# Kernel optimization log

Measured on AMD Instinct MI355X. Metric: run time of the kernel, lower is better.

## Reference

```python
import jax, jax.numpy as jnp
import numpy as np

HIDDEN = 1024
ATTN = 1024
B, L = 16, 1024


def setup_inputs() -> dict:
    key = jax.random.key(0)
    ks = jax.random.split(key, 9)
    s = 1.0 / np.sqrt(HIDDEN)
    return {
        "meme_features": jax.random.normal(ks[0], (B, L, HIDDEN), jnp.float32),
        "text_features": jax.random.normal(ks[1], (B, L, HIDDEN), jnp.float32),
        "emoji_features": jax.random.normal(ks[2], (B, L, HIDDEN), jnp.float32),
        # nn.Linear params: weight [out, in], bias [out]
        "Wq": jax.random.uniform(ks[3], (ATTN, HIDDEN), jnp.float32, -s, s),
        "bq": jax.random.uniform(ks[4], (ATTN,), jnp.float32, -s, s),
        "Wk": jax.random.uniform(ks[5], (ATTN, HIDDEN), jnp.float32, -s, s),
        "bk": jax.random.uniform(ks[6], (ATTN,), jnp.float32, -s, s),
        "Wv": jax.random.uniform(ks[7], (ATTN, HIDDEN), jnp.float32, -s, s),
        "bv": jax.random.uniform(ks[8], (ATTN,), jnp.float32, -s, s),
    }


def reference(meme_features, text_features, emoji_features, Wq, bq, Wk, bk, Wv, bv):
    # Linear projections (x @ W^T + b)
    q = jnp.einsum("blh,ah->bla", meme_features, Wq) + bq   # [B, Lq, A]
    k = jnp.einsum("blh,ah->bla", text_features, Wk) + bk   # [B, Lk, A]
    v = jnp.einsum("blh,ah->bla", emoji_features, Wv) + bv  # [B, Lk, A]
    # NOTE: original module has NO 1/sqrt(d) scaling and NO mask.
    scores = jnp.einsum("bqa,bka->bqk", q, k)               # [B, Lq, Lk]
    weights = jax.nn.softmax(scores, axis=-1)
    return jnp.einsum("bqk,bka->bqa", weights, v)           # [B, Lq, A]
```

## Files before the change

### kernel.cpp

```cpp
#include <hip/hip_runtime.h>

typedef _Float16 half8_t __attribute__((ext_vector_type(8)));
typedef _Float16 half4_t __attribute__((ext_vector_type(4)));
typedef float floatx4 __attribute__((ext_vector_type(4)));

__device__ inline void gload16(const void* g, void* l) {
  __builtin_amdgcn_global_load_lds(
      (const __attribute__((address_space(1))) unsigned int*)g,
      (__attribute__((address_space(3))) unsigned int*)l, 16, 0, 0);
}

constexpr int NT = 16;

template <int MH>
__device__ inline void lda_frags(const char* sA, int wr, int quad, int mrow,
                                 half8_t af[4][2]) {
#pragma unroll
  for (int mf = 0; mf < 4; ++mf)
#pragma unroll
    for (int kk = 0; kk < 2; ++kk)
      af[mf][kk] = *(const half8_t*)(
          sA + (size_t)(((kk * 4 + quad) * 256 + MH * 128 + wr * 64 +
                         mf * 16 + mrow) << 4));
}

template <int NH>
__device__ inline void ldb_frags(const char* sB, int wc, int quad, int mrow,
                                 half8_t bf[2][2]) {
#pragma unroll
  for (int nf = 0; nf < 2; ++nf)
#pragma unroll
    for (int kk = 0; kk < 2; ++kk)
      bf[nf][kk] = *(const half8_t*)(
          sB + (size_t)(((kk * 4 + quad) * 256 + NH * 128 + wc * 32 +
                         nf * 16 + mrow) << 4));
}

template <int MH, int NH>
__device__ inline void mfma_quad(const half8_t af[4][2], const half8_t bf[2][2],
                                 floatx4 acc[8][4]) {
  __builtin_amdgcn_s_setprio(1);
#pragma unroll
  for (int mf = 0; mf < 4; ++mf)
#pragma unroll
    for (int nf = 0; nf < 2; ++nf)
#pragma unroll
      for (int kk = 0; kk < 2; ++kk)
        acc[MH * 4 + mf][NH * 2 + nf] = __builtin_amdgcn_mfma_f32_16x16x32_f16(
            af[mf][kk], bf[nf][kk], acc[MH * 4 + mf][NH * 2 + nf], 0, 0, 0);
  __builtin_amdgcn_s_setprio(0);
}

__device__ inline void stage_half(const _Float16* __restrict__ X, int ldx,
                                  int u, char* opbase, int h, int wid,
                                  int lane) {
#pragma unroll
  for (int i = 0; i < 2; ++i) {
    gload16(X + (long)(h * 128 + i * 64 + lane) * ldx + u * 64 + wid * 8,
            opbase + (size_t)((wid * 256 + h * 128 + i * 64) << 4));
  }
}

template <typename OT, int BIAS, int GX, int GY>
__global__ __launch_bounds__(512, 2) void gemm256(
    const _Float16* __restrict__ A, long As, int lda,
    const _Float16* __restrict__ B, long Bs, int ldb,
    OT* __restrict__ C, long Cs, int ldc,
    const float* __restrict__ bias, int biasStride) {
  __shared__ char smem[131072];

  const int id = blockIdx.x;
  const int chunk = gridDim.x >> 3;
  const int nid = (id & 7) * chunk + (id >> 3);
  const int bx = nid % GX;
  const int by = (nid / GX) % GY;
  const int bz = nid / (GX * GY);

  const int tid = threadIdx.x;
  const int lane = tid & 63;
  const int wid = tid >> 6;
  const int wr = wid >> 2;
  const int wc = wid & 3;
  const int quad = lane >> 4;
  const int mrow = lane & 15;
  const long m0 = (long)by * 256;
  const long n0 = (long)bx * 256;
  const _Float16* Ab = A + (long)bz * As + m0 * (long)lda;
  const _Float16* Bb = B + (long)bz * Bs + n0 * (long)ldb;
  C += (long)bz * Cs;

  floatx4 acc[8][4] = {};
  half8_t af[4][2], bf[2][2];

  {
    char* sA0 = smem;
    char* sB0 = smem + 65536;
    char* sA1 = smem + 32768;
    char* sB1 = smem + 65536 + 32768;
    stage_half(Ab, lda, 0, sA0, 0, wid, lane);
    stage_half(Bb, ldb, 0, sB0, 1, wid, lane);
    stage_half(Ab, lda, 0, sA0, 1, wid, lane);
    stage_half(Bb, ldb, 0, sB0, 0, wid, lane);
    stage_half(Ab, lda, 1, sA1, 0, wid, lane);
    stage_half(Bb, ldb, 1, sB1, 1, wid, lane);
    stage_half(Ab, lda, 1, sA1, 1, wid, lane);
    asm volatile("s_waitcnt vmcnt(6)" ::: "memory");
    __builtin_amdgcn_s_barrier();
  }

  for (int t = 0; t < NT; ++t) {
    const int p = t & 1, q = p ^ 1;
    char* sAp = smem + p * 32768;
    char* sBp = smem + 65536 + p * 32768;
    char* sBq = smem + 65536 + q * 32768;
    const int u1 = (t + 1 < NT) ? t + 1 : NT - 1;
    const int u2 = (t + 2 < NT) ? t + 2 : NT - 1;

    lda_frags<0>(sAp, wr, quad, mrow, af);
    ldb_frags<0>(sBp, wc, quad, mrow, bf);
    stage_half(Bb, ldb, u1, sBq, 0, wid, lane);
    __builtin_amdgcn_s_barrier();
    asm volatile("s_waitcnt lgkmcnt(0)" ::: "memory");
    mfma_quad<0, 0>(af, bf, acc);
    __builtin_amdgcn_s_barrier();

    ldb_frags<1>(sBp, wc, quad, mrow, bf);
    stage_half(Ab, lda, u2, sAp, 0, wid, lane);
    __builtin_amdgcn_s_barrier();
    asm volatile("s_waitcnt lgkmcnt(0)" ::: "memory");
    mfma_quad<0, 1>(af, bf, acc);
    __builtin_amdgcn_s_barrier();

    lda_frags<1>(sAp, wr, quad, mrow, af);
    stage_half(Bb, ldb, u2, sBp, 1, wid, lane);
    __builtin_amdgcn_s_barrier();
    asm volatile("s_waitcnt lgkmcnt(0)" ::: "memory");
    mfma_quad<1, 1>(af, bf, acc);
    __builtin_amdgcn_s_barrier();

    ldb_frags<0>(sBp, wc, quad, mrow, bf);
    stage_half(Ab, lda, u2, sAp, 1, wid, lane);
    asm volatile("s_waitcnt vmcnt(6)" ::: "memory");
    __builtin_amdgcn_s_barrier();
    asm volatile("s_waitcnt lgkmcnt(0)" ::: "memory");
    mfma_quad<1, 0>(af, bf, acc);
    __builtin_amdgcn_s_barrier();
  }

  asm volatile("s_waitcnt vmcnt(0)" ::: "memory");

#pragma unroll
  for (int mh = 0; mh < 2; ++mh)
#pragma unroll
    for (int mf = 0; mf < 4; ++mf) {
      const int rbase = mh * 128 + wr * 64 + mf * 16 + quad * 4;
#pragma unroll
      for (int nh = 0; nh < 2; ++nh)
#pragma unroll
        for (int nf = 0; nf < 2; ++nf) {
          const int cc = (int)n0 + nh * 128 + wc * 32 + nf * 16 + mrow;
#pragma unroll
          for (int r = 0; r < 4; ++r) {
            const long row = m0 + rbase + r;
            float v = acc[mh * 4 + mf][nh * 2 + nf][r];
            if constexpr (BIAS == 1) v += bias[bz * biasStride + cc];
            if constexpr (BIAS == 2) v += bias[(int)row];
            C[row * (long)ldc + cc] = (OT)v;
          }
        }
    }
}


__global__ __launch_bounds__(256) void convert_x(const float* __restrict__ x0,
                                                 const float* __restrict__ x1,
                                                 const float* __restrict__ x2,
                                                 _Float16* __restrict__ out) {
  int i = blockIdx.x * 256 + threadIdx.x;
  int t = i >> 22;
  int j = i & 4194303;
  const float* src = (t == 0) ? x0 : (t == 1) ? x1 : x2;
  floatx4 v = ((const floatx4*)src)[j];
  half4_t h = {(_Float16)v[0], (_Float16)v[1], (_Float16)v[2], (_Float16)v[3]};
  ((half4_t*)out)[i] = h;
}

__global__ __launch_bounds__(256) void convert_w(const float* __restrict__ Wq,
                                                 const float* __restrict__ Wk,
                                                 const float* __restrict__ Wv,
                                                 _Float16* __restrict__ out) {
  int i = blockIdx.x * 256 + threadIdx.x;
  int t = i >> 18;
  int j = i & 262143;
  const float* src = (t == 0) ? Wq : (t == 1) ? Wk : Wv;
  floatx4 v = ((const floatx4*)src)[j];
  half4_t h = {(_Float16)v[0], (_Float16)v[1], (_Float16)v[2], (_Float16)v[3]};
  ((half4_t*)out)[i] = h;
}

__global__ __launch_bounds__(256) void pack_bias(const float* __restrict__ bq,
                                                 const float* __restrict__ bk,
                                                 const float* __restrict__ bv,
                                                 float* __restrict__ out) {
  int b = blockIdx.x;
  const float* src = (b == 0) ? bq : (b == 1) ? bk : bv;
  ((floatx4*)out)[b * 256 + threadIdx.x] =
      ((const floatx4*)src)[threadIdx.x];
}

__global__ __launch_bounds__(256) void softmax_rows_h(_Float16* __restrict__ S) {
  long row = blockIdx.x;
  _Float16* Sr = S + row * 1024;
  int tid = threadIdx.x, lane = tid & 63, wid = tid >> 6;
  half4_t x = ((const half4_t*)Sr)[tid];
  float x0 = x[0], x1 = x[1], x2 = x[2], x3 = x[3];
  float mx = fmaxf(fmaxf(x0, x1), fmaxf(x2, x3));
#pragma unroll
  for (int off = 32; off > 0; off >>= 1) mx = fmaxf(mx, __shfl_xor(mx, off));
  __shared__ float redm[4];
  if (lane == 0) redm[wid] = mx;
  __syncthreads();
  mx = fmaxf(fmaxf(redm[0], redm[1]), fmaxf(redm[2], redm[3]));
  float e0 = __expf(x0 - mx), e1 = __expf(x1 - mx);
  float e2 = __expf(x2 - mx), e3 = __expf(x3 - mx);
  float s = e0 + e1 + e2 + e3;
#pragma unroll
  for (int off = 32; off > 0; off >>= 1) s += __shfl_xor(s, off);
  __shared__ float reds[4];
  if (lane == 0) reds[wid] = s;
  __syncthreads();
  s = reds[0] + reds[1] + reds[2] + reds[3];
  float inv = 1.0f / s;
  half4_t h = {(_Float16)(e0 * inv), (_Float16)(e1 * inv),
               (_Float16)(e2 * inv), (_Float16)(e3 * inv)};
  ((half4_t*)Sr)[tid] = h;
}

extern "C" void kernel_launch(void* const* d_in, const int* in_sizes, int n_in,
                              void* d_out, int out_size, void* d_ws,
                              size_t ws_size, hipStream_t stream) {
  (void)in_sizes; (void)n_in; (void)out_size; (void)ws_size;
  const float* meme  = (const float*)d_in[0];
  const float* text  = (const float*)d_in[1];
  const float* emoji = (const float*)d_in[2];
  const float* Wq = (const float*)d_in[3];
  const float* bq = (const float*)d_in[4];
  const float* Wk = (const float*)d_in[5];
  const float* bk = (const float*)d_in[6];
  const float* Wv = (const float*)d_in[7];
  const float* bv = (const float*)d_in[8];

  const long MB = 1024 * 1024;
  char* ws = (char*)d_ws;
  _Float16* hWq = (_Float16*)ws;
  float* pbias  = (float*)(ws + 6 * MB);
  _Float16* mh  = (_Float16*)(ws + 7 * MB);
  _Float16* th  = (_Float16*)(ws + 39 * MB);
  _Float16* eh  = (_Float16*)(ws + 71 * MB);
  _Float16* Qh  = (_Float16*)(ws + 103 * MB);
  _Float16* Kh  = (_Float16*)(ws + 135 * MB);
  _Float16* S   = mh;
  _Float16* Vt  = th;
  _Float16* hWv = hWq + 2 * MB;

  dim3 blk(256), blk5(512);
  convert_w<<<3072, blk, 0, stream>>>(Wq, Wk, Wv, hWq);
  pack_bias<<<3, blk, 0, stream>>>(bq, bk, bv, pbias);
  convert_x<<<49152, blk, 0, stream>>>(meme, text, emoji, mh);

  gemm256<_Float16, 1, 4, 64><<<dim3(512), blk5, 0, stream>>>(
      mh, 16777216, 1024, hWq, 1048576, 1024, Qh, 16777216, 1024, pbias, 1024);
  gemm256<_Float16, 2, 64, 4><<<dim3(256), blk5, 0, stream>>>(
      hWv, 0, 1024, eh, 0, 1024, Vt, 0, 16384, pbias + 2048, 0);
  gemm256<_Float16, 0, 4, 4><<<dim3(256), blk5, 0, stream>>>(
      Qh, 1048576, 1024, Kh, 1048576, 1024, S, 1048576, 1024, nullptr, 0);
  softmax_rows_h<<<16384, blk, 0, stream>>>(S);
  gemm256<float, 0, 4, 4><<<dim3(256), blk5, 0, stream>>>(
      S, 1048576, 1024, Vt, 1024, 16384, (float*)d_out, 1048576, 1024,
      nullptr, 0);
}
```

Before: 472.6 us.

## Software-pipeline GEMM main loop with per-k-half fragments and fewer barriers

```diff
diff --git a/kernel.cpp b/kernel.cpp
--- a/kernel.cpp
+++ b/kernel.cpp
@@ -12,42 +12,34 @@
 
 constexpr int NT = 16;
 
-template <int MH>
-__device__ inline void lda_frags(const char* sA, int wr, int quad, int mrow,
-                                 half8_t af[4][2]) {
+__device__ inline void lda1(const char* sA, int kk, int qm, int wr, int quad,
+                            int mrow, half8_t af[4]) {
 #pragma unroll
   for (int mf = 0; mf < 4; ++mf)
-#pragma unroll
-    for (int kk = 0; kk < 2; ++kk)
-      af[mf][kk] = *(const half8_t*)(
-          sA + (size_t)(((kk * 4 + quad) * 256 + MH * 128 + wr * 64 +
-                         mf * 16 + mrow) << 4));
-}
-
-template <int NH>
-__device__ inline void ldb_frags(const char* sB, int wc, int quad, int mrow,
-                                 half8_t bf[2][2]) {
+    af[mf] = *(const half8_t*)(
+        sA + (size_t)(((kk * 4 + quad) * 256 + qm * 128 + wr * 64 + mf * 16 +
+                       mrow) << 4));
+}
+
+__device__ inline void ldb1(const char* sB, int kk, int qn, int wc, int quad,
+                            int mrow, half8_t bf[2]) {
 #pragma unroll
   for (int nf = 0; nf < 2; ++nf)
-#pragma unroll
-    for (int kk = 0; kk < 2; ++kk)
-      bf[nf][kk] = *(const half8_t*)(
-          sB + (size_t)(((kk * 4 + quad) * 256 + NH * 128 + wc * 32 +
-                         nf * 16 + mrow) << 4));
-}
-
-template <int MH, int NH>
-__device__ inline void mfma_quad(const half8_t af[4][2], const half8_t bf[2][2],
-                                 floatx4 acc[8][4]) {
+    bf[nf] = *(const half8_t*)(
+        sB + (size_t)(((kk * 4 + quad) * 256 + qn * 128 + wc * 32 + nf * 16 +
+                       mrow) << 4));
+}
+
+template <int QM, int QN>
+__device__ inline void mfma8(const half8_t af[4], const half8_t bf[2],
+                             floatx4 acc[8][4]) {
   __builtin_amdgcn_s_setprio(1);
 #pragma unroll
   for (int mf = 0; mf < 4; ++mf)
 #pragma unroll
     for (int nf = 0; nf < 2; ++nf)
-#pragma unroll
-      for (int kk = 0; kk < 2; ++kk)
-        acc[MH * 4 + mf][NH * 2 + nf] = __builtin_amdgcn_mfma_f32_16x16x32_f16(
-            af[mf][kk], bf[nf][kk], acc[MH * 4 + mf][NH * 2 + nf], 0, 0, 0);
+      acc[QM * 4 + mf][QN * 2 + nf] = __builtin_amdgcn_mfma_f32_16x16x32_f16(
+          af[mf], bf[nf], acc[QM * 4 + mf][QN * 2 + nf], 0, 0, 0);
   __builtin_amdgcn_s_setprio(0);
 }
 
@@ -90,7 +82,7 @@
   C += (long)bz * Cs;
 
   floatx4 acc[8][4] = {};
-  half8_t af[4][2], bf[2][2];
+  half8_t af_a[4], af_b[4], bfA[2], bfB[2];
 
   {
     char* sA0 = smem;
@@ -98,53 +90,55 @@
     char* sA1 = smem + 32768;
     char* sB1 = smem + 65536 + 32768;
     stage_half(Ab, lda, 0, sA0, 0, wid, lane);
-    stage_half(Bb, ldb, 0, sB0, 1, wid, lane);
     stage_half(Ab, lda, 0, sA0, 1, wid, lane);
     stage_half(Bb, ldb, 0, sB0, 0, wid, lane);
+    stage_half(Bb, ldb, 0, sB0, 1, wid, lane);
     stage_half(Ab, lda, 1, sA1, 0, wid, lane);
+    stage_half(Ab, lda, 1, sA1, 1, wid, lane);
+    stage_half(Bb, ldb, 1, sB1, 0, wid, lane);
     stage_half(Bb, ldb, 1, sB1, 1, wid, lane);
-    stage_half(Ab, lda, 1, sA1, 1, wid, lane);
-    asm volatile("s_waitcnt vmcnt(6)" ::: "memory");
-    __builtin_amdgcn_s_barrier();
+    asm volatile("s_waitcnt vmcnt(8)" ::: "memory");
+    __builtin_amdgcn_s_barrier();
+    lda1(sA0, 0, 0, wr, quad, mrow, af_a);
+    ldb1(sB0, 0, 0, wc, quad, mrow, bfA);
   }
 
   for (int t = 0; t < NT; ++t) {
     const int p = t & 1, q = p ^ 1;
-    char* sAp = smem + p * 32768;
-    char* sBp = smem + 65536 + p * 32768;
-    char* sBq = smem + 65536 + q * 32768;
-    const int u1 = (t + 1 < NT) ? t + 1 : NT - 1;
-    const int u2 = (t + 2 < NT) ? t + 2 : NT - 1;
-
-    lda_frags<0>(sAp, wr, quad, mrow, af);
-    ldb_frags<0>(sBp, wc, quad, mrow, bf);
-    stage_half(Bb, ldb, u1, sBq, 0, wid, lane);
-    __builtin_amdgcn_s_barrier();
+    char* sAc = smem + p * 32768;
+    char* sBc = smem + 65536 + p * 32768;
+    char* sAn = smem + q * 32768;
+    char* sBn = smem + 65536 + q * 32768;
+    const int tu = (t + 2 < NT) ? t + 2 : NT - 1;
+
+    ldb1(sBc, 0, 1, wc, quad, mrow, bfB);
+    mfma8<0, 0>(af_a, bfA, acc);
+    lda1(sAc, 0, 1, wr, quad, mrow, af_b);
+    mfma8<0, 1>(af_a, bfB, acc);
+    mfma8<1, 1>(af_b, bfB, acc);
+    lda1(sAc, 1, 1, wr, quad, mrow, af_a);
+    ldb1(sBc, 1, 0, wc, quad, mrow, bfB);
+    mfma8<1, 0>(af_b, bfA, acc);
     asm volatile("s_waitcnt lgkmcnt(0)" ::: "memory");
-    mfma_quad<0, 0>(af, bf, acc);
-    __builtin_amdgcn_s_barrier();
-
-    ldb_frags<1>(sBp, wc, quad, mrow, bf);
-    stage_half(Ab, lda, u2, sAp, 0, wid, lane);
-    __builtin_amdgcn_s_barrier();
+    __builtin_amdgcn_s_barrier();
+    stage_half(Ab, lda, tu, sAc, 1, wid, lane);
+    stage_half(Bb, ldb, tu, sBc, 0, wid, lane);
+    ldb1(sBc, 1, 1, wc, quad, mrow, bfA);
+    mfma8<1, 0>(af_a, bfB, acc);
     asm volatile("s_waitcnt lgkmcnt(0)" ::: "memory");
-    mfma_quad<0, 1>(af, bf, acc);
-    __builtin_amdgcn_s_barrier();
-
-    lda_frags<1>(sAp, wr, quad, mrow, af);
-    stage_half(Bb, ldb, u2, sBp, 1, wid, lane);
-    __builtin_amdgcn_s_barrier();
+    __builtin_amdgcn_s_barrier();
+    stage_half(Bb, ldb, tu, sBc, 1, wid, lane);
+    lda1(sAc, 1, 0, wr, quad, mrow, af_b);
+    mfma8<1, 1>(af_a, bfA, acc);
     asm volatile("s_waitcnt lgkmcnt(0)" ::: "memory");
-    mfma_quad<1, 1>(af, bf, acc);
-    __builtin_amdgcn_s_barrier();
-
-    ldb_frags<0>(sBp, wc, quad, mrow, bf);
-    stage_half(Ab, lda, u2, sAp, 1, wid, lane);
-    asm volatile("s_waitcnt vmcnt(6)" ::: "memory");
-    __builtin_amdgcn_s_barrier();
-    asm volatile("s_waitcnt lgkmcnt(0)" ::: "memory");
-    mfma_quad<1, 0>(af, bf, acc);
-    __builtin_amdgcn_s_barrier();
+    __builtin_amdgcn_s_barrier();
+    stage_half(Ab, lda, tu, sAc, 0, wid, lane);
+    mfma8<0, 1>(af_b, bfA, acc);
+    asm volatile("s_waitcnt vmcnt(8)" ::: "memory");
+    __builtin_amdgcn_s_barrier();
+    lda1(sAn, 0, 0, wr, quad, mrow, af_a);
+    ldb1(sBn, 0, 0, wc, quad, mrow, bfA);
+    mfma8<0, 0>(af_b, bfB, acc);
   }
 
   asm volatile("s_waitcnt vmcnt(0)" ::: "memory");
```

Result: slower. 482.3 us (+2.0%).

## Fuse fp32-to-fp16 conversion of Q/K inputs into GEMM and switch to 32x32 MFMA

Applied to the files above, without the earlier changes.

```diff
diff --git a/kernel.cpp b/kernel.cpp
--- a/kernel.cpp
+++ b/kernel.cpp
@@ -3,6 +3,7 @@
 typedef _Float16 half8_t __attribute__((ext_vector_type(8)));
 typedef _Float16 half4_t __attribute__((ext_vector_type(4)));
 typedef float floatx4 __attribute__((ext_vector_type(4)));
+typedef float f32x16 __attribute__((ext_vector_type(16)));
 
 __device__ inline void gload16(const void* g, void* l) {
   __builtin_amdgcn_global_load_lds(
@@ -13,41 +14,36 @@
 constexpr int NT = 16;
 
 template <int MH>
-__device__ inline void lda_frags(const char* sA, int wr, int quad, int mrow,
-                                 half8_t af[4][2]) {
-#pragma unroll
-  for (int mf = 0; mf < 4; ++mf)
-#pragma unroll
-    for (int kk = 0; kk < 2; ++kk)
-      af[mf][kk] = *(const half8_t*)(
-          sA + (size_t)(((kk * 4 + quad) * 256 + MH * 128 + wr * 64 +
-                         mf * 16 + mrow) << 4));
+__device__ inline void lda_frags(const char* sA, int wr, int lo, int hi,
+                                 half8_t af[2][4]) {
+#pragma unroll
+  for (int mp = 0; mp < 2; ++mp)
+#pragma unroll
+    for (int ks = 0; ks < 4; ++ks)
+      af[mp][ks] = *(const half8_t*)(
+          sA + (size_t)(((ks * 2 + hi) * 256 + MH * 128 + wr * 64 + mp * 32 +
+                         lo) << 4));
 }
 
 template <int NH>
-__device__ inline void ldb_frags(const char* sB, int wc, int quad, int mrow,
-                                 half8_t bf[2][2]) {
-#pragma unroll
-  for (int nf = 0; nf < 2; ++nf)
-#pragma unroll
-    for (int kk = 0; kk < 2; ++kk)
-      bf[nf][kk] = *(const half8_t*)(
-          sB + (size_t)(((kk * 4 + quad) * 256 + NH * 128 + wc * 32 +
-                         nf * 16 + mrow) << 4));
-}
-
-template <int MH, int NH>
-__device__ inline void mfma_quad(const half8_t af[4][2], const half8_t bf[2][2],
-                                 floatx4 acc[8][4]) {
+__device__ inline void ldb_frags(const char* sB, int wc, int lo, int hi,
+                                 half8_t bf[4]) {
+#pragma unroll
+  for (int ks = 0; ks < 4; ++ks)
+    bf[ks] = *(const half8_t*)(
+        sB + (size_t)(((ks * 2 + hi) * 256 + NH * 128 + wc * 32 + lo) << 4));
+}
+
+template <int MQ, int NI>
+__device__ inline void mfma_quad(const half8_t af[2][4], const half8_t bf[4],
+                                 f32x16 acc[4][2]) {
   __builtin_amdgcn_s_setprio(1);
 #pragma unroll
-  for (int mf = 0; mf < 4; ++mf)
-#pragma unroll
-    for (int nf = 0; nf < 2; ++nf)
-#pragma unroll
-      for (int kk = 0; kk < 2; ++kk)
-        acc[MH * 4 + mf][NH * 2 + nf] = __builtin_amdgcn_mfma_f32_16x16x32_f16(
-            af[mf][kk], bf[nf][kk], acc[MH * 4 + mf][NH * 2 + nf], 0, 0, 0);
+  for (int mp = 0; mp < 2; ++mp)
+#pragma unroll
+    for (int ks = 0; ks < 4; ++ks)
+      acc[MQ + mp][NI] = __builtin_amdgcn_mfma_f32_32x32x16_f16(
+          af[mp][ks], bf[ks], acc[MQ + mp][NI], 0, 0, 0);
   __builtin_amdgcn_s_setprio(0);
 }
 
@@ -61,12 +57,38 @@
   }
 }
 
-template <typename OT, int BIAS, int GX, int GY>
+__device__ inline void a32_issue(const float* __restrict__ X, int ldx, int u,
+                                 int wid, int lane, floatx4 va[4][2]) {
+#pragma unroll
+  for (int hj = 0; hj < 4; ++hj) {
+    const float* src =
+        X + (long)((hj >> 1) * 128 + (hj & 1) * 64 + lane) * ldx + u * 64 +
+        wid * 8;
+    va[hj][0] = *(const floatx4*)(src);
+    va[hj][1] = *(const floatx4*)(src + 4);
+  }
+}
+
+__device__ inline void a32_write(char* opbase, int wid, int lane,
+                                 const floatx4 va[4][2]) {
+#pragma unroll
+  for (int hj = 0; hj < 4; ++hj) {
+    half8_t h = {(_Float16)va[hj][0][0], (_Float16)va[hj][0][1],
+                 (_Float16)va[hj][0][2], (_Float16)va[hj][0][3],
+                 (_Float16)va[hj][1][0], (_Float16)va[hj][1][1],
+                 (_Float16)va[hj][1][2], (_Float16)va[hj][1][3]};
+    *(half8_t*)(opbase +
+                (size_t)((wid * 256 + (hj >> 1) * 128 + (hj & 1) * 64 + lane)
+                         << 4)) = h;
+  }
+}
+
+template <typename OT, int BIAS, int GX, int GY, int ACVT>
 __global__ __launch_bounds__(512, 2) void gemm256(
-    const _Float16* __restrict__ A, long As, int lda,
-    const _Float16* __restrict__ B, long Bs, int ldb,
-    OT* __restrict__ C, long Cs, int ldc,
-    const float* __restrict__ bias, int biasStride) {
+    const _Float16* __restrict__ A, const float* __restrict__ A32, long As,
+    int lda, const _Float16* __restrict__ B, long Bs, int ldb,
+    OT* __restrict__ C, long Cs, int ldc, const float* __restrict__ bias,
+    int biasStride) {
   __shared__ char smem[131072];
 
   const int id = blockIdx.x;
@@ -81,22 +103,38 @@
   const int wid = tid >> 6;
   const int wr = wid >> 2;
   const int wc = wid & 3;
-  const int quad = lane >> 4;
-  const int mrow = lane & 15;
+  const int lo = lane & 31;
+  const int hi = lane >> 5;
   const long m0 = (long)by * 256;
   const long n0 = (long)bx * 256;
-  const _Float16* Ab = A + (long)bz * As + m0 * (long)lda;
+  const _Float16* Ab = A;
+  const float* A32b = A32;
+  if constexpr (ACVT) A32b += (long)bz * As + m0 * (long)lda;
+  else Ab += (long)bz * As + m0 * (long)lda;
   const _Float16* Bb = B + (long)bz * Bs + n0 * (long)ldb;
   C += (long)bz * Cs;
 
-  floatx4 acc[8][4] = {};
-  half8_t af[4][2], bf[2][2];
-
-  {
-    char* sA0 = smem;
-    char* sB0 = smem + 65536;
-    char* sA1 = smem + 32768;
-    char* sB1 = smem + 65536 + 32768;
+  f32x16 acc[4][2] = {};
+  half8_t af[2][4], bf0[4], bf1[4];
+  floatx4 va[4][2];
+
+  char* sA0 = smem;
+  char* sA1 = smem + 32768;
+  char* sB0 = smem + 65536;
+  char* sB1 = smem + 65536 + 32768;
+
+  if constexpr (ACVT) {
+    a32_issue(A32b, lda, 0, wid, lane, va);
+    stage_half(Bb, ldb, 0, sB0, 0, wid, lane);
+    stage_half(Bb, ldb, 0, sB0, 1, wid, lane);
+    stage_half(Bb, ldb, 1, sB1, 1, wid, lane);
+    asm volatile("s_waitcnt vmcnt(6)" ::: "memory");
+    a32_write(sA0, wid, lane, va);
+    a32_issue(A32b, lda, 1, wid, lane, va);
+    asm volatile("s_waitcnt vmcnt(0)" ::: "memory");
+    a32_write(sA1, wid, lane, va);
+    __syncthreads();
+  } else {
     stage_half(Ab, lda, 0, sA0, 0, wid, lane);
     stage_half(Bb, ldb, 0, sB0, 1, wid, lane);
     stage_half(Ab, lda, 0, sA0, 1, wid, lane);
@@ -110,77 +148,75 @@
 
   for (int t = 0; t < NT; ++t) {
     const int p = t & 1, q = p ^ 1;
-    char* sAp = smem + p * 32768;
-    char* sBp = smem + 65536 + p * 32768;
+    char* sAc = smem + p * 32768;
+    char* sBc = smem + 65536 + p * 32768;
     char* sBq = smem + 65536 + q * 32768;
     const int u1 = (t + 1 < NT) ? t + 1 : NT - 1;
     const int u2 = (t + 2 < NT) ? t + 2 : NT - 1;
 
-    lda_frags<0>(sAp, wr, quad, mrow, af);
-    ldb_frags<0>(sBp, wc, quad, mrow, bf);
+    lda_frags<0>(sAc, wr, lo, hi, af);
+    ldb_frags<0>(sBc, wc, lo, hi, bf0);
     stage_half(Bb, ldb, u1, sBq, 0, wid, lane);
     __builtin_amdgcn_s_barrier();
     asm volatile("s_waitcnt lgkmcnt(0)" ::: "memory");
-    mfma_quad<0, 0>(af, bf, acc);
-    __builtin_amdgcn_s_barrier();
-
-    ldb_frags<1>(sBp, wc, quad, mrow, bf);
-    stage_half(Ab, lda, u2, sAp, 0, wid, lane);
+    mfma_quad<0, 0>(af, bf0, acc);
+    __builtin_amdgcn_s_barrier();
+
+    ldb_frags<1>(sBc, wc, lo, hi, bf1);
+    if constexpr (ACVT)
+      a32_issue(A32b, lda, u2, wid, lane, va);
+    else
+      stage_half(Ab, lda, u2, sAc, 0, wid, lane);
     __builtin_amdgcn_s_barrier();
     asm volatile("s_waitcnt lgkmcnt(0)" ::: "memory");
-    mfma_quad<0, 1>(af, bf, acc);
-    __builtin_amdgcn_s_barrier();
-
-    lda_frags<1>(sAp, wr, quad, mrow, af);
-    stage_half(Bb, ldb, u2, sBp, 1, wid, lane);
+    mfma_quad<0, 1>(af, bf1, acc);
+    __builtin_amdgcn_s_barrier();
+
+    lda_frags<1>(sAc, wr, lo, hi, af);
+    stage_half(Bb, ldb, u2, sBc, 1, wid, lane);
     __builtin_amdgcn_s_barrier();
     asm volatile("s_waitcnt lgkmcnt(0)" ::: "memory");
-    mfma_quad<1, 1>(af, bf, acc);
-    __builtin_amdgcn_s_barrier();
-
-    ldb_frags<0>(sBp, wc, quad, mrow, bf);
-    stage_half(Ab, lda, u2, sAp, 1, wid, lane);
-    asm volatile("s_waitcnt vmcnt(6)" ::: "memory");
+    mfma_quad<2, 1>(af, bf1, acc);
+    __builtin_amdgcn_s_barrier();
+
+    if constexpr (ACVT) {
+      asm volatile("s_waitcnt vmcnt(2)" ::: "memory");
+      a32_write(sAc, wid, lane, va);
+    } else {
+      stage_half(Ab, lda, u2, sAc, 1, wid, lane);
+      asm volatile("s_waitcnt vmcnt(6)" ::: "memory");
+    }
     __builtin_amdgcn_s_barrier();
     asm volatile("s_waitcnt lgkmcnt(0)" ::: "memory");
-    mfma_quad<1, 0>(af, bf, acc);
+    mfma_quad<2, 0>(af, bf0, acc);
     __builtin_amdgcn_s_barrier();
   }
 
   asm volatile("s_waitcnt vmcnt(0)" ::: "memory");
 
 #pragma unroll
-  for (int mh = 0; mh < 2; ++mh)
-#pragma unroll
-    for (int mf = 0; mf < 4; ++mf) {
-      const int rbase = mh * 128 + wr * 64 + mf * 16 + quad * 4;
-#pragma unroll
-      for (int nh = 0; nh < 2; ++nh)
-#pragma unroll
-        for (int nf = 0; nf < 2; ++nf) {
-          const int cc = (int)n0 + nh * 128 + wc * 32 + nf * 16 + mrow;
-#pragma unroll
-          for (int r = 0; r < 4; ++r) {
-            const long row = m0 + rbase + r;
-            float v = acc[mh * 4 + mf][nh * 2 + nf][r];
-            if constexpr (BIAS == 1) v += bias[bz * biasStride + cc];
-            if constexpr (BIAS == 2) v += bias[(int)row];
-            C[row * (long)ldc + cc] = (OT)v;
-          }
-        }
+  for (int mi = 0; mi < 4; ++mi) {
+    const int r0 = (mi >> 1) * 128 + wr * 64 + (mi & 1) * 32 + 4 * hi;
+#pragma unroll
+    for (int ni = 0; ni < 2; ++ni) {
+      const int cc = (int)n0 + ni * 128 + wc * 32 + lo;
+#pragma unroll
+      for (int e = 0; e < 16; ++e) {
+        const long row = m0 + r0 + (e & 3) + 8 * (e >> 2);
+        float v = acc[mi][ni][e];
+        if constexpr (BIAS == 1) v += bias[bz * biasStride + cc];
+        if constexpr (BIAS == 2) v += bias[(int)row];
+        C[row * (long)ldc + cc] = (OT)v;
+      }
     }
-}
-
-
-__global__ __launch_bounds__(256) void convert_x(const float* __restrict__ x0,
-                                                 const float* __restrict__ x1,
-                                                 const float* __restrict__ x2,
+  }
+}
+
+
+__global__ __launch_bounds__(256) void convert_e(const float* __restrict__ x,
                                                  _Float16* __restrict__ out) {
   int i = blockIdx.x * 256 + threadIdx.x;
-  int t = i >> 22;
-  int j = i & 4194303;
-  const float* src = (t == 0) ? x0 : (t == 1) ? x1 : x2;
-  floatx4 v = ((const floatx4*)src)[j];
+  floatx4 v = ((const floatx4*)x)[i];
   half4_t h = {(_Float16)v[0], (_Float16)v[1], (_Float16)v[2], (_Float16)v[3]};
   ((half4_t*)out)[i] = h;
 }
@@ -254,28 +290,30 @@
   char* ws = (char*)d_ws;
   _Float16* hWq = (_Float16*)ws;
   float* pbias  = (float*)(ws + 6 * MB);
-  _Float16* mh  = (_Float16*)(ws + 7 * MB);
-  _Float16* th  = (_Float16*)(ws + 39 * MB);
+  _Float16* S   = (_Float16*)(ws + 7 * MB);
+  _Float16* Vt  = (_Float16*)(ws + 39 * MB);
   _Float16* eh  = (_Float16*)(ws + 71 * MB);
   _Float16* Qh  = (_Float16*)(ws + 103 * MB);
   _Float16* Kh  = (_Float16*)(ws + 135 * MB);
-  _Float16* S   = mh;
-  _Float16* Vt  = th;
+  _Float16* hWk = hWq + 1 * MB;
   _Float16* hWv = hWq + 2 * MB;
 
   dim3 blk(256), blk5(512);
   convert_w<<<3072, blk, 0, stream>>>(Wq, Wk, Wv, hWq);
   pack_bias<<<3, blk, 0, stream>>>(bq, bk, bv, pbias);
-  convert_x<<<49152, blk, 0, stream>>>(meme, text, emoji, mh);
-
-  gemm256<_Float16, 1, 4, 64><<<dim3(512), blk5, 0, stream>>>(
-      mh, 16777216, 1024, hWq, 1048576, 1024, Qh, 16777216, 1024, pbias, 1024);
-  gemm256<_Float16, 2, 64, 4><<<dim3(256), blk5, 0, stream>>>(
-      hWv, 0, 1024, eh, 0, 1024, Vt, 0, 16384, pbias + 2048, 0);
-  gemm256<_Float16, 0, 4, 4><<<dim3(256), blk5, 0, stream>>>(
-      Qh, 1048576, 1024, Kh, 1048576, 1024, S, 1048576, 1024, nullptr, 0);
+  convert_e<<<16384, blk, 0, stream>>>(emoji, eh);
+
+  gemm256<_Float16, 1, 4, 64, 1><<<dim3(256), blk5, 0, stream>>>(
+      nullptr, meme, 0, 1024, hWq, 0, 1024, Qh, 0, 1024, pbias, 0);
+  gemm256<_Float16, 1, 4, 64, 1><<<dim3(256), blk5, 0, stream>>>(
+      nullptr, text, 0, 1024, hWk, 0, 1024, Kh, 0, 1024, pbias + 1024, 0);
+  gemm256<_Float16, 2, 64, 4, 0><<<dim3(256), blk5, 0, stream>>>(
+      hWv, nullptr, 0, 1024, eh, 0, 1024, Vt, 0, 16384, pbias + 2048, 0);
+  gemm256<_Float16, 0, 4, 4, 0><<<dim3(256), blk5, 0, stream>>>(
+      Qh, nullptr, 1048576, 1024, Kh, 1048576, 1024, S, 1048576, 1024,
+      nullptr, 0);
   softmax_rows_h<<<16384, blk, 0, stream>>>(S);
-  gemm256<float, 0, 4, 4><<<dim3(256), blk5, 0, stream>>>(
-      S, 1048576, 1024, Vt, 1024, 16384, (float*)d_out, 1048576, 1024,
-      nullptr, 0);
-}
+  gemm256<float, 0, 4, 4, 0><<<dim3(256), blk5, 0, stream>>>(
+      S, nullptr, 1048576, 1024, Vt, 1024, 16384, (float*)d_out, 1048576,
+      1024, nullptr, 0);
+}
```

Result: slower. 509.0 us (+7.7%).

## Switch GEMM to 32x32x16 MFMA with XOR-swizzled LDS layout

Applied to the files above, without the earlier changes.

```diff
diff --git a/kernel.cpp b/kernel.cpp
--- a/kernel.cpp
+++ b/kernel.cpp
@@ -3,6 +3,7 @@
 typedef _Float16 half8_t __attribute__((ext_vector_type(8)));
 typedef _Float16 half4_t __attribute__((ext_vector_type(4)));
 typedef float floatx4 __attribute__((ext_vector_type(4)));
+typedef float f32x16 __attribute__((ext_vector_type(16)));
 
 __device__ inline void gload16(const void* g, void* l) {
   __builtin_amdgcn_global_load_lds(
@@ -12,52 +13,44 @@
 
 constexpr int NT = 16;
 
-template <int MH>
-__device__ inline void lda_frags(const char* sA, int wr, int quad, int mrow,
-                                 half8_t af[4][2]) {
-#pragma unroll
-  for (int mf = 0; mf < 4; ++mf)
-#pragma unroll
-    for (int kk = 0; kk < 2; ++kk)
-      af[mf][kk] = *(const half8_t*)(
-          sA + (size_t)(((kk * 4 + quad) * 256 + MH * 128 + wr * 64 +
-                         mf * 16 + mrow) << 4));
-}
-
-template <int NH>
-__device__ inline void ldb_frags(const char* sB, int wc, int quad, int mrow,
-                                 half8_t bf[2][2]) {
-#pragma unroll
-  for (int nf = 0; nf < 2; ++nf)
-#pragma unroll
-    for (int kk = 0; kk < 2; ++kk)
-      bf[nf][kk] = *(const half8_t*)(
-          sB + (size_t)(((kk * 4 + quad) * 256 + NH * 128 + wc * 32 +
-                         nf * 16 + mrow) << 4));
-}
-
-template <int MH, int NH>
-__device__ inline void mfma_quad(const half8_t af[4][2], const half8_t bf[2][2],
-                                 floatx4 acc[8][4]) {
+__device__ inline void lda_frags2(const char* sA, int rb, const int* xk,
+                                  half8_t af[2][4]) {
+#pragma unroll
+  for (int mp = 0; mp < 2; ++mp)
+#pragma unroll
+    for (int ks = 0; ks < 4; ++ks)
+      af[mp][ks] = *(const half8_t*)(
+          sA + (size_t)((rb + mp * 32) * 128 + xk[ks] * 16));
+}
+
+__device__ inline void ldb_frags2(const char* sB, int cb, const int* xk,
+                                  half8_t bf[4]) {
+#pragma unroll
+  for (int ks = 0; ks < 4; ++ks)
+    bf[ks] = *(const half8_t*)(sB + (size_t)(cb * 128 + xk[ks] * 16));
+}
+
+template <int MQ, int NI>
+__device__ inline void mfma_quad(const half8_t af[2][4], const half8_t bf[4],
+                                 f32x16 acc[4][2]) {
   __builtin_amdgcn_s_setprio(1);
 #pragma unroll
-  for (int mf = 0; mf < 4; ++mf)
-#pragma unroll
-    for (int nf = 0; nf < 2; ++nf)
-#pragma unroll
-      for (int kk = 0; kk < 2; ++kk)
-        acc[MH * 4 + mf][NH * 2 + nf] = __builtin_amdgcn_mfma_f32_16x16x32_f16(
-            af[mf][kk], bf[nf][kk], acc[MH * 4 + mf][NH * 2 + nf], 0, 0, 0);
+  for (int mp = 0; mp < 2; ++mp)
+#pragma unroll
+    for (int ks = 0; ks < 4; ++ks)
+      acc[MQ + mp][NI] = __builtin_amdgcn_mfma_f32_32x32x16_f16(
+          af[mp][ks], bf[ks], acc[MQ + mp][NI], 0, 0, 0);
   __builtin_amdgcn_s_setprio(0);
 }
 
-__device__ inline void stage_half(const _Float16* __restrict__ X, int ldx,
-                                  int u, char* opbase, int h, int wid,
-                                  int lane) {
+__device__ inline void stage_half(const _Float16* __restrict__ X, long laneoff,
+                                  int ldx, int u, char* opbase, int h,
+                                  int wid) {
 #pragma unroll
   for (int i = 0; i < 2; ++i) {
-    gload16(X + (long)(h * 128 + i * 64 + lane) * ldx + u * 64 + wid * 8,
-            opbase + (size_t)((wid * 256 + h * 128 + i * 64) << 4));
+    const int c0 = h * 1024 + wid * 128 + i * 64;
+    gload16(X + (long)(c0 >> 3) * ldx + u * 64 + laneoff,
+            opbase + (size_t)c0 * 16);
   }
 }
 
@@ -65,8 +58,8 @@
 __global__ __launch_bounds__(512, 2) void gemm256(
     const _Float16* __restrict__ A, long As, int lda,
     const _Float16* __restrict__ B, long Bs, int ldb,
-    OT* __restrict__ C, long Cs, int ldc,
-    const float* __restrict__ bias, int biasStride) {
+    OT* __restrict__ C, long Cs, int ldc, const float* __restrict__ bias,
+    int biasStride) {
   __shared__ char smem[131072];
 
   const int id = blockIdx.x;
@@ -81,94 +74,96 @@
   const int wid = tid >> 6;
   const int wr = wid >> 2;
   const int wc = wid & 3;
-  const int quad = lane >> 4;
-  const int mrow = lane & 15;
+  const int lo = lane & 31;
+  const int hi = lane >> 5;
+  const int l7 = lane & 7;
+  const int l8 = lane >> 3;
+  const long laneA = (long)l8 * lda + ((l7 ^ l8) << 3);
+  const long laneB = (long)l8 * ldb + ((l7 ^ l8) << 3);
+  int xk[4];
+#pragma unroll
+  for (int ks = 0; ks < 4; ++ks) xk[ks] = (ks * 2 + hi) ^ l7;
+
   const long m0 = (long)by * 256;
   const long n0 = (long)bx * 256;
   const _Float16* Ab = A + (long)bz * As + m0 * (long)lda;
   const _Float16* Bb = B + (long)bz * Bs + n0 * (long)ldb;
   C += (long)bz * Cs;
 
-  floatx4 acc[8][4] = {};
-  half8_t af[4][2], bf[2][2];
-
-  {
-    char* sA0 = smem;
-    char* sB0 = smem + 65536;
-    char* sA1 = smem + 32768;
-    char* sB1 = smem + 65536 + 32768;
-    stage_half(Ab, lda, 0, sA0, 0, wid, lane);
-    stage_half(Bb, ldb, 0, sB0, 1, wid, lane);
-    stage_half(Ab, lda, 0, sA0, 1, wid, lane);
-    stage_half(Bb, ldb, 0, sB0, 0, wid, lane);
-    stage_half(Ab, lda, 1, sA1, 0, wid, lane);
-    stage_half(Bb, ldb, 1, sB1, 1, wid, lane);
-    stage_half(Ab, lda, 1, sA1, 1, wid, lane);
-    asm volatile("s_waitcnt vmcnt(6)" ::: "memory");
-    __builtin_amdgcn_s_barrier();
-  }
+  f32x16 acc[4][2] = {};
+  half8_t af[2][4], bf0[4], bf1[4];
+
+  char* sA0 = smem;
+  char* sA1 = smem + 32768;
+  char* sB0 = smem + 65536;
+  char* sB1 = smem + 65536 + 32768;
+
+  stage_half(Ab, laneA, lda, 0, sA0, 0, wid);
+  stage_half(Bb, laneB, ldb, 0, sB0, 1, wid);
+  stage_half(Ab, laneA, lda, 0, sA0, 1, wid);
+  stage_half(Bb, laneB, ldb, 0, sB0, 0, wid);
+  stage_half(Ab, laneA, lda, 1, sA1, 0, wid);
+  stage_half(Bb, laneB, ldb, 1, sB1, 1, wid);
+  stage_half(Ab, laneA, lda, 1, sA1, 1, wid);
+  asm volatile("s_waitcnt vmcnt(6)" ::: "memory");
+  __builtin_amdgcn_s_barrier();
 
   for (int t = 0; t < NT; ++t) {
     const int p = t & 1, q = p ^ 1;
-    char* sAp = smem + p * 32768;
-    char* sBp = smem + 65536 + p * 32768;
+    char* sAc = smem + p * 32768;
+    char* sBc = smem + 65536 + p * 32768;
     char* sBq = smem + 65536 + q * 32768;
     const int u1 = (t + 1 < NT) ? t + 1 : NT - 1;
     const int u2 = (t + 2 < NT) ? t + 2 : NT - 1;
 
-    lda_frags<0>(sAp, wr, quad, mrow, af);
-    ldb_frags<0>(sBp, wc, quad, mrow, bf);
-    stage_half(Bb, ldb, u1, sBq, 0, wid, lane);
-    __builtin_amdgcn_s_barrier();
-    asm volatile("s_waitcnt lgkmcnt(0)" ::: "memory");
-    mfma_quad<0, 0>(af, bf, acc);
-    __builtin_amdgcn_s_barrier();
-
-    ldb_frags<1>(sBp, wc, quad, mrow, bf);
-    stage_half(Ab, lda, u2, sAp, 0, wid, lane);
-    __builtin_amdgcn_s_barrier();
-    asm volatile("s_waitcnt lgkmcnt(0)" ::: "memory");
-    mfma_quad<0, 1>(af, bf, acc);
-    __builtin_amdgcn_s_barrier();
-
-    lda_frags<1>(sAp, wr, quad, mrow, af);
-    stage_half(Bb, ldb, u2, sBp, 1, wid, lane);
-    __builtin_amdgcn_s_barrier();
-    asm volatile("s_waitcnt lgkmcnt(0)" ::: "memory");
-    mfma_quad<1, 1>(af, bf, acc);
-    __builtin_amdgcn_s_barrier();
-
-    ldb_frags<0>(sBp, wc, quad, mrow, bf);
-    stage_half(Ab, lda, u2, sAp, 1, wid, lane);
+    lda_frags2(sAc, wr * 64 + lo, xk, af);
+    ldb_frags2(sBc, wc * 32 + lo, xk, bf0);
+    stage_half(Bb, laneB, ldb, u1, sBq, 0, wid);
+    __builtin_amdgcn_s_barrier();
+    asm volatile("s_waitcnt lgkmcnt(0)" ::: "memory");
+    mfma_quad<0, 0>(af, bf0, acc);
+    __builtin_amdgcn_s_barrier();
+
+    ldb_frags2(sBc, 128 + wc * 32 + lo, xk, bf1);
+    stage_half(Ab, laneA, lda, u2, sAc, 0, wid);
+    __builtin_amdgcn_s_barrier();
+    asm volatile("s_waitcnt lgkmcnt(0)" ::: "memory");
+    mfma_quad<0, 1>(af, bf1, acc);
+    __builtin_amdgcn_s_barrier();
+
+    lda_frags2(sAc, 128 + wr * 64 + lo, xk, af);
+    stage_half(Bb, laneB, ldb, u2, sBc, 1, wid);
+    __builtin_amdgcn_s_barrier();
+    asm volatile("s_waitcnt lgkmcnt(0)" ::: "memory");
+    mfma_quad<2, 1>(af, bf1, acc);
+    __builtin_amdgcn_s_barrier();
+
+    stage_half(Ab, laneA, lda, u2, sAc, 1, wid);
     asm volatile("s_waitcnt vmcnt(6)" ::: "memory");
     __builtin_amdgcn_s_barrier();
     asm volatile("s_waitcnt lgkmcnt(0)" ::: "memory");
-    mfma_quad<1, 0>(af, bf, acc);
+    mfma_quad<2, 0>(af, bf0, acc);
     __builtin_amdgcn_s_barrier();
   }
 
   asm volatile("s_waitcnt vmcnt(0)" ::: "memory");
 
 #pragma unroll
-  for (int mh = 0; mh < 2; ++mh)
-#pragma unroll
-    for (int mf = 0; mf < 4; ++mf) {
-      const int rbase = mh * 128 + wr * 64 + mf * 16 + quad * 4;
-#pragma unroll
-      for (int nh = 0; nh < 2; ++nh)
-#pragma unroll
-        for (int nf = 0; nf < 2; ++nf) {
-          const int cc = (int)n0 + nh * 128 + wc * 32 + nf * 16 + mrow;
-#pragma unroll
-          for (int r = 0; r < 4; ++r) {
-            const long row = m0 + rbase + r;
-            float v = acc[mh * 4 + mf][nh * 2 + nf][r];
-            if constexpr (BIAS == 1) v += bias[bz * biasStride + cc];
-            if constexpr (BIAS == 2) v += bias[(int)row];
-            C[row * (long)ldc + cc] = (OT)v;
-          }
-        }
+  for (int mi = 0; mi < 4; ++mi) {
+    const int r0 = (mi >> 1) * 128 + wr * 64 + (mi & 1) * 32 + 4 * hi;
+#pragma unroll
+    for (int ni = 0; ni < 2; ++ni) {
+      const int cc = (int)n0 + ni * 128 + wc * 32 + lo;
+#pragma unroll
+      for (int e = 0; e < 16; ++e) {
+        const long row = m0 + r0 + (e & 3) + 8 * (e >> 2);
+        float v = acc[mi][ni][e];
+        if constexpr (BIAS == 1) v += bias[bz * biasStride + cc];
+        if constexpr (BIAS == 2) v += bias[(int)row];
+        C[row * (long)ldc + cc] = (OT)v;
+      }
     }
+  }
 }
 
 
```

Result: faster. 444.9 us (-5.9%).
